# Kernel tuning notes

Hardware: AMD Instinct MI355X
Metric: run time of the kernel (lower is better)

The kernel has to match this reference:

```python
import jax, jax.numpy as jnp
import numpy as np

B, L, DIN = 2, 4096, 1024
W = 64            # windowsize
G, H = 8, 8       # groups, heads per group
DQ = DV = 64
FF = 1024
NEG = -1e30


def rmsnorm(x, gamma, d):
    # F.normalize(x, dim=-1) * sqrt(d) * gamma
    n = jnp.sqrt(jnp.sum(x * x, axis=-1, keepdims=True))
    return x / jnp.maximum(n, 1e-12) * (d ** 0.5) * gamma


def setup_inputs() -> dict:
    key = jax.random.key(0)
    ks = jax.random.split(key, 8)
    s = 0.02
    return {
        "x": jax.random.normal(ks[0], (B, L, DIN), jnp.float32),
        "norm_gamma": jnp.ones((DIN,), jnp.float32),
        "Wq_w": jax.random.normal(ks[1], (G * H * DQ, DIN), jnp.float32) * s,
        "Wq_b": jnp.zeros((G * H * DQ,), jnp.float32),
        "Wkv_w": jax.random.normal(ks[2], (G * (DQ + DV), DIN), jnp.float32) * s,
        "Wkv_b": jnp.zeros((G * (DQ + DV),), jnp.float32),
        "wz_gamma1": jnp.ones((G * H * DV,), jnp.float32),
        "W1_w": jax.random.normal(ks[3], (2 * FF, G * H * DV), jnp.float32) * s,
        "W1_b": jnp.zeros((2 * FF,), jnp.float32),
        "wz_gamma2": jnp.ones((2 * FF,), jnp.float32),
        "W2_w": jax.random.normal(ks[4], (FF, 2 * FF), jnp.float32) * s,
        "W2_b": jnp.zeros((FF,), jnp.float32),
    }


def reference(x, norm_gamma, Wq_w, Wq_b, Wkv_w, Wkv_b,
              wz_gamma1, W1_w, W1_b, wz_gamma2, W2_w, W2_b):
    w2, w4 = W // 2, W // 4
    S = 2 * L // W  # number of query chunks (L % W == 0 -> drop_last path)

    xn = rmsnorm(x, norm_gamma, DIN)
    q = xn @ Wq_w.T + Wq_b          # [B, L, G*H*DQ]
    kv = xn @ Wkv_w.T + Wkv_b       # [B, L, G*(DQ+DV)]

    # pad_to_multiple(kv, W, mod=W//2): L % W == 0 -> append W//2 zeros
    kv = jnp.pad(kv, ((0, 0), (0, w2), (0, 0)))
    k, v = jnp.split(kv, 2, axis=-1)  # each [B, L+W/2, G*DQ]
    # F.pad W//4 both sides, then overlapping windows of size W, stride W//2
    k = jnp.pad(k, ((0, 0), (w4, w4), (0, 0)))  # [B, L+W, G*DQ]
    v = jnp.pad(v, ((0, 0), (w4, w4), (0, 0)))
    idx = jnp.arange(S)[:, None] * w2 + jnp.arange(W)[None, :]  # [S, W] (drop_last applied)
    kwin = k[:, idx].reshape(B, S, W, G, DQ).transpose(0, 3, 1, 2, 4)  # [B,G,S,W,DQ]
    vwin = v[:, idx].reshape(B, S, W, G, DV).transpose(0, 3, 1, 2, 4)  # [B,G,S,W,DV]

    # 'B (S w) (G H D) -> B G H S w D'
    qh = q.reshape(B, S, w2, G, H, DQ).transpose(0, 3, 4, 1, 2, 5)  # [B,G,H,S,w2,DQ]

    qk = jnp.einsum('bghsqd,bgskd->bghsqk', qh, kwin) * (1.0 / DQ ** 0.5)
    # edge masking: first chunk can't see left pad, last chunk can't see right pad
    maskb = jnp.zeros((S, W), bool).at[0, :w4].set(True).at[S - 1, W - w4:].set(True)
    qk = jnp.where(maskb[None, None, None, :, None, :], NEG, qk)
    attn = jax.nn.softmax(qk, axis=-1)
    o = jnp.einsum('bghsqk,bgskd->bghsqd', attn, vwin)
    o = o.transpose(0, 3, 4, 1, 2, 5).reshape(B, L, G * H * DV)  # 'B G H S w D -> B (S w) (G H D)'

    # Wz: RMSNorm -> Linear -> SiLU -> RMSNorm -> Linear -> SiLU (dropout=0)
    z = rmsnorm(o, wz_gamma1, G * H * DV)
    z = jax.nn.silu(z @ W1_w.T + W1_b)
    z = rmsnorm(z, wz_gamma2, 2 * FF)
    z = jax.nn.silu(z @ W2_w.T + W2_b)
    return z
```

## Files before the change

### kernel.cpp

```cpp
#include <hip/hip_runtime.h>
#include <cstdint>

typedef _Float16 f16;
typedef f16 f16x4 __attribute__((ext_vector_type(4)));
typedef f16 f16x8 __attribute__((ext_vector_type(8)));
typedef float f32x4 __attribute__((ext_vector_type(4)));

#define MFMA16(a, b, c) __builtin_amdgcn_mfma_f32_16x16x32_f16(a, b, c, 0, 0, 0)

static __device__ __forceinline__ void gload16(const void* g, void* l) {
    __builtin_amdgcn_global_load_lds(
        (const __attribute__((address_space(1))) uint32_t*)g,
        (__attribute__((address_space(3))) uint32_t*)l, 16, 0, 0);
}

template <int NM, int ND, int NV>
static __device__ __forceinline__ void sgb_phase() {
    if (NV > 0) __builtin_amdgcn_sched_group_barrier(0x10, NV, 0);
    constexpr int PER = NM / ND;
#pragma unroll
    for (int i = 0; i < ND; ++i) {
        __builtin_amdgcn_sched_group_barrier(0x8, PER, 0);
        __builtin_amdgcn_sched_group_barrier(0x100, 1, 0);
    }
    if (NM - PER * ND > 0)
        __builtin_amdgcn_sched_group_barrier(0x8, NM - PER * ND, 0);
}

static __device__ __forceinline__ float blockReduceSum256(float v) {
    __shared__ float red[4];
#pragma unroll
    for (int off = 32; off > 0; off >>= 1) v += __shfl_xor(v, off);
    if ((threadIdx.x & 63) == 0) red[threadIdx.x >> 6] = v;
    __syncthreads();
    return red[0] + red[1] + red[2] + red[3];
}

__global__ __launch_bounds__(256) void k_rmsnorm_x(const float* __restrict__ x,
                                                   const float* __restrict__ gamma,
                                                   f16* __restrict__ out) {
    size_t row = blockIdx.x;
    const float4 v = reinterpret_cast<const float4*>(x + row * 1024)[threadIdx.x];
    float ss = v.x * v.x + v.y * v.y + v.z * v.z + v.w * v.w;
    ss = blockReduceSum256(ss);
    float sc = 32.0f / fmaxf(sqrtf(ss), 1e-12f);
    const float4 g = reinterpret_cast<const float4*>(gamma)[threadIdx.x];
    f16x4 o;
    o[0] = (f16)(v.x * sc * g.x); o[1] = (f16)(v.y * sc * g.y);
    o[2] = (f16)(v.z * sc * g.z); o[3] = (f16)(v.w * sc * g.w);
    *reinterpret_cast<f16x4*>(out + row * 1024 + threadIdx.x * 4) = o;
}

template <int D>
__global__ __launch_bounds__(256) void k_rowss(const f16* __restrict__ in,
                                               float* __restrict__ sc) {
    constexpr int PER = D / 256;
    size_t row = blockIdx.x;
    const f16* ir = in + row * D;
    int c0 = threadIdx.x * PER;
    float ss = 0.f;
#pragma unroll
    for (int i = 0; i < PER; i += 8) {
        f16x8 h = *reinterpret_cast<const f16x8*>(ir + c0 + i);
#pragma unroll
        for (int e = 0; e < 8; ++e) { float f = (float)h[e]; ss += f * f; }
    }
    ss = blockReduceSum256(ss);
    if (threadIdx.x == 0)
        sc[row] = sqrtf((float)D) / fmaxf(sqrtf(ss), 1e-12f);
}

__global__ __launch_bounds__(256) void k_cast(const float* __restrict__ in,
                                              f16* __restrict__ out, int n4) {
    int i = blockIdx.x * 256 + threadIdx.x;
    if (i >= n4) return;
    float4 v = reinterpret_cast<const float4*>(in)[i];
    f16x4 o; o[0] = (f16)v.x; o[1] = (f16)v.y; o[2] = (f16)v.z; o[3] = (f16)v.w;
    *reinterpret_cast<f16x4*>(out + (size_t)i * 4) = o;
}

__global__ __launch_bounds__(256) void k_cast_g(const float* __restrict__ in,
                                                f16* __restrict__ out,
                                                const float* __restrict__ gamma,
                                                int kmask, int n4) {
    int i = blockIdx.x * 256 + threadIdx.x;
    if (i >= n4) return;
    float4 v = reinterpret_cast<const float4*>(in)[i];
    int e0 = (i * 4) & kmask;
    f16x4 o;
    o[0] = (f16)(v.x * gamma[e0]); o[1] = (f16)(v.y * gamma[e0 + 1]);
    o[2] = (f16)(v.z * gamma[e0 + 2]); o[3] = (f16)(v.w * gamma[e0 + 3]);
    *reinterpret_cast<f16x4*>(out + (size_t)i * 4) = o;
}

__global__ __launch_bounds__(256) void k_bias_cat(const float* __restrict__ a,
                                                  const float* __restrict__ b,
                                                  float* __restrict__ o) {
    int i = blockIdx.x * 256 + threadIdx.x;
    o[i] = (i < 4096) ? a[i] : b[i - 4096];
}

template <int BN, int EPI, int MODE>
__global__ __launch_bounds__(512, 2) void k_gemm8p(const f16* __restrict__ A,
                                                   const f16* __restrict__ Bt,
                                                   const float* __restrict__ bias,
                                                   const float* __restrict__ rowsc,
                                                   void* __restrict__ Cout,
                                                   int M, int N, int K) {
    constexpr int BM = 256;
    constexpr int WN = BN / 64, WM = 8 / WN, WR = BM / WM;
    constexpr int MW = WR / 16, MH = MW / 2;
    constexpr int LA = 2, LB = BN / 128;
    constexpr int VS = 2 * LA + LB;
    constexpr int AK = BM * 32;
    constexpr int BKE = BN * 32;
    constexpr int SE = 2 * AK + 2 * BKE;

    __shared__ alignas(16) f16 lds[2 * SE];

    const int nb = N / BN;
    int bn, bm;
    if (MODE == 0) { bn = blockIdx.x & 7; bm = blockIdx.x >> 3; }
    else           { bn = blockIdx.x % nb; bm = blockIdx.x / nb; }

    const int tid = threadIdx.x, w = tid >> 6, l = tid & 63;
    const int wm = w / WN, wn = w % WN;
    const int lrow = l & 15, lq = l >> 4;
    const int g = (lrow >> 1) & 3;

    const f16* Ab = A + (size_t)bm * BM * K;
    const f16* Bb = Bt + (size_t)bn * BN * K;
    const int NT = K >> 6;

    int aoff[MW], boff[4];
#pragma unroll
    for (int m = 0; m < MW; ++m)
        aoff[m] = (wm * WR + m * 16 + lrow) * 32 + 8 * (lq ^ g);
#pragma unroll
    for (int n = 0; n < 4; ++n)
        boff[n] = (wn * 64 + n * 16 + lrow) * 32 + 8 * (lq ^ g);

    auto stageA = [&](int k0, f16* region) {
#pragma unroll
        for (int q = 0; q < LA; ++q) {
            int r = q * 128 + w * 16 + (l >> 2);
            int c = 8 * ((l & 3) ^ ((r >> 1) & 3));
            gload16(Ab + (size_t)r * K + k0 + c, region + q * 4096 + w * 512);
        }
    };
    auto stageB = [&](int k0, f16* region) {
#pragma unroll
        for (int q = 0; q < LB; ++q) {
            int r = q * 128 + w * 16 + (l >> 2);
            int c = 8 * ((l & 3) ^ ((r >> 1) & 3));
            gload16(Bb + (size_t)r * K + k0 + c, region + q * 4096 + w * 512);
        }
    };
    auto rdA = [&](f16x8 (&d)[MH], const f16* base, int h) {
#pragma unroll
        for (int m = 0; m < MH; ++m)
            d[m] = *reinterpret_cast<const f16x8*>(base + aoff[h * MH + m]);
    };
    auto rdB = [&](f16x8 (&d)[4], const f16* base) {
#pragma unroll
        for (int n = 0; n < 4; ++n)
            d[n] = *reinterpret_cast<const f16x8*>(base + boff[n]);
    };

    f32x4 acc[MW][4] = {};
    f16x8 afA[MH], afB[MH], bfA[4], bfB[4];

    auto mfmaLo = [&](f16x8 (&af)[MH], f16x8 (&bf)[4]) {
#pragma unroll
        for (int m = 0; m < MH; ++m)
#pragma unroll
            for (int n = 0; n < 4; ++n)
                acc[m][n] = MFMA16(af[m], bf[n], acc[m][n]);
    };
    auto mfmaHi = [&](f16x8 (&af)[MH], f16x8 (&bf)[4]) {
#pragma unroll
        for (int m = 0; m < MH; ++m)
#pragma unroll
            for (int n = 0; n < 4; ++n)
                acc[MH + m][n] = MFMA16(af[m], bf[n], acc[MH + m][n]);
    };

    stageA(0, lds);             stageB(0, lds + 2 * AK);
    stageA(32, lds + AK);       stageB(32, lds + 2 * AK + BKE);
    stageA(64, lds + SE);       stageB(64, lds + SE + 2 * AK);
    asm volatile("s_waitcnt vmcnt(%0)" :: "i"(2 * (LA + LB)) : "memory");
    __builtin_amdgcn_s_barrier();
    rdA(afA, lds, 0);
    rdB(bfA, lds + 2 * AK);

    const int NTm2 = NT - 2;
    for (int t = 0; t < NTm2; ++t) {
        f16* s0 = lds + (t & 1) * SE;
        f16* s1 = lds + ((t & 1) ^ 1) * SE;
        const int kn1 = (t + 1) << 6;
        const int kn2 = (t + 2) << 6;
        __builtin_amdgcn_s_barrier();
        stageA(kn1 + 32, s1 + AK);
        rdA(afB, s0, 1);
        mfmaLo(afA, bfA);
        sgb_phase<MH * 4, MH, LA>();
        asm volatile("s_waitcnt vmcnt(%0)" :: "i"(VS) : "memory");
        __builtin_amdgcn_s_barrier();
        stageB(kn1 + 32, s1 + 2 * AK + BKE);
        rdA(afA, s0 + AK, 0);
        rdB(bfB, s0 + 2 * AK + BKE);
        mfmaHi(afB, bfA);
        sgb_phase<MH * 4, MH + 4, LB>();
        __builtin_amdgcn_s_barrier();
        stageA(kn2, s0);
        rdA(afB, s0 + AK, 1);
        mfmaLo(afA, bfB);
        sgb_phase<MH * 4, MH, LA>();
        asm volatile("s_waitcnt vmcnt(%0)" :: "i"(VS) : "memory");
        __builtin_amdgcn_s_barrier();
        stageB(kn2, s0 + 2 * AK);
        rdA(afA, s1, 0);
        rdB(bfA, s1 + 2 * AK);
        mfmaHi(afB, bfB);
        sgb_phase<MH * 4, MH + 4, LB>();
    }
    {
        const int t = NTm2;
        f16* s0 = lds + (t & 1) * SE;
        f16* s1 = lds + ((t & 1) ^ 1) * SE;
        const int kn1 = (t + 1) << 6;
        __builtin_amdgcn_s_barrier();
        stageA(kn1 + 32, s1 + AK);
        rdA(afB, s0, 1);
        mfmaLo(afA, bfA);
        sgb_phase<MH * 4, MH, LA>();
        asm volatile("s_waitcnt vmcnt(%0)" :: "i"(VS) : "memory");
        __builtin_amdgcn_s_barrier();
        stageB(kn1 + 32, s1 + 2 * AK + BKE);
        rdA(afA, s0 + AK, 0);
        rdB(bfB, s0 + 2 * AK + BKE);
        mfmaHi(afB, bfA);
        sgb_phase<MH * 4, MH + 4, LB>();
        __builtin_amdgcn_s_barrier();
        rdA(afB, s0 + AK, 1);
        mfmaLo(afA, bfB);
        sgb_phase<MH * 4, MH, 0>();
        asm volatile("s_waitcnt vmcnt(%0)" :: "i"(LA + LB) : "memory");
        __builtin_amdgcn_s_barrier();
        rdA(afA, s1, 0);
        rdB(bfA, s1 + 2 * AK);
        mfmaHi(afB, bfB);
        sgb_phase<MH * 4, MH + 4, 0>();
    }
    {
        f16* s0 = lds + ((NT - 1) & 1) * SE;
        __builtin_amdgcn_s_barrier();
        rdA(afB, s0, 1);
        mfmaLo(afA, bfA);
        sgb_phase<MH * 4, MH, 0>();
        asm volatile("s_waitcnt vmcnt(0)" ::: "memory");
        __builtin_amdgcn_s_barrier();
        rdA(afA, s0 + AK, 0);
        rdB(bfB, s0 + 2 * AK + BKE);
        mfmaHi(afB, bfA);
        sgb_phase<MH * 4, MH + 4, 0>();
        __builtin_amdgcn_s_barrier();
        rdA(afB, s0 + AK, 1);
        mfmaLo(afA, bfB);
        sgb_phase<MH * 4, MH, 0>();
        mfmaHi(afB, bfB);
    }

    const size_t row0 = (size_t)bm * BM + wm * WR;
    const int col0 = bn * BN + wn * 64;
    float bsv[4];
#pragma unroll
    for (int n = 0; n < 4; ++n) bsv[n] = bias[col0 + n * 16 + lrow];
#pragma unroll
    for (int m = 0; m < MW; ++m) {
#pragma unroll
        for (int r = 0; r < 4; ++r) {
            const size_t row = row0 + m * 16 + lq * 4 + r;
            float scl = (EPI >= 1) ? rowsc[row] : 1.0f;
#pragma unroll
            for (int n = 0; n < 4; ++n) {
                float v = acc[m][n][r];
                if (EPI >= 1) v = v * scl;
                v += bsv[n];
                if (EPI >= 1) v = v / (1.f + __expf(-v));
                const size_t idx = row * N + col0 + n * 16 + lrow;
                if (EPI == 2) reinterpret_cast<float*>(Cout)[idx] = v;
                else          reinterpret_cast<f16*>(Cout)[idx] = (f16)v;
            }
        }
    }
}

__global__ __launch_bounds__(256) void k_attn(const f16* __restrict__ qkv,
                                              f16* __restrict__ o) {
    __shared__ alignas(16) f16 Ksm[64 * 64];
    __shared__ alignas(16) f16 Vtsm[64 * 64];
    __shared__ alignas(16) f16 Psm[4][64 * 64];
    const int idx = blockIdx.x;
    const int s = idx & 127;
    const int g = (idx >> 7) & 7;
    const int b = idx >> 10;
    const int tid = threadIdx.x;
    const int w = tid >> 6, l = tid & 63;

    const int baseR = s * 32 - 16;
#pragma unroll
    for (int i = 0; i < 2; ++i) {
        const int j = i * 32 + (tid >> 3);
        const int d0 = (tid & 7) * 8;
        const int R = baseR + j;
        f16x8 kvv = {}, vvv = {};
        if (R >= 0 && R < 4096) {
            const f16* rp = qkv + ((size_t)(b * 4096 + R)) * 5120 + 4096 + g * 64 + d0;
            kvv = *reinterpret_cast<const f16x8*>(rp);
            vvv = *reinterpret_cast<const f16x8*>(rp + 512);
        }
        *reinterpret_cast<f16x8*>(&Ksm[j * 64 + d0]) = kvv;
#pragma unroll
        for (int e = 0; e < 8; ++e) Vtsm[(d0 + e) * 64 + j] = vvv[e];
    }

    const int lrow = l & 15, lk = (l >> 4) * 8;
    f16x8 aq[4][2];
#pragma unroll
    for (int m = 0; m < 4; ++m) {
        const int qr = w * 64 + m * 16 + lrow;
        const int h = qr >> 5, qi = qr & 31;
        const f16* qp = qkv + ((size_t)(b * 4096 + s * 32 + qi)) * 5120 + (g * 8 + h) * 64 + lk;
        aq[m][0] = *reinterpret_cast<const f16x8*>(qp);
        aq[m][1] = *reinterpret_cast<const f16x8*>(qp + 32);
    }
    __syncthreads();

    f32x4 acc[4][4] = {};
#pragma unroll
    for (int kk = 0; kk < 2; ++kk) {
        f16x8 bk[4];
#pragma unroll
        for (int n = 0; n < 4; ++n)
            bk[n] = *reinterpret_cast<const f16x8*>(&Ksm[(n * 16 + lrow) * 64 + kk * 32 + lk]);
#pragma unroll
        for (int m = 0; m < 4; ++m)
#pragma unroll
            for (int n = 0; n < 4; ++n)
                acc[m][n] = MFMA16(aq[m][kk], bk[n], acc[m][n]);
    }

    const int nlo = (s == 0) ? 1 : 0;
    const int nhi = (s == 127) ? 3 : 4;
#pragma unroll
    for (int m = 0; m < 4; ++m) {
#pragma unroll
        for (int r = 0; r < 4; ++r) {
            float xv[4];
#pragma unroll
            for (int n = 0; n < 4; ++n) xv[n] = acc[m][n][r] * 0.125f;
            float mx = -1e30f;
            for (int n = nlo; n < nhi; ++n) mx = fmaxf(mx, xv[n]);
#pragma unroll
            for (int off = 8; off > 0; off >>= 1) mx = fmaxf(mx, __shfl_xor(mx, off));
            float pv[4]; float sum = 0.f;
#pragma unroll
            for (int n = 0; n < 4; ++n) {
                float e = (n >= nlo && n < nhi) ? __expf(xv[n] - mx) : 0.f;
                pv[n] = e; sum += e;
            }
#pragma unroll
            for (int off = 8; off > 0; off >>= 1) sum += __shfl_xor(sum, off);
            const float inv = 1.f / sum;
            const int prow = m * 16 + (l >> 4) * 4 + r;
#pragma unroll
            for (int n = 0; n < 4; ++n)
                Psm[w][prow * 64 + n * 16 + lrow] = (f16)(pv[n] * inv);
        }
    }
    __syncthreads();

    f32x4 oacc[4][4] = {};
#pragma unroll
    for (int kk = 0; kk < 2; ++kk) {
        f16x8 ap[4], bv[4];
#pragma unroll
        for (int m = 0; m < 4; ++m)
            ap[m] = *reinterpret_cast<const f16x8*>(&Psm[w][(m * 16 + lrow) * 64 + kk * 32 + lk]);
#pragma unroll
        for (int n = 0; n < 4; ++n)
            bv[n] = *reinterpret_cast<const f16x8*>(&Vtsm[(n * 16 + lrow) * 64 + kk * 32 + lk]);
#pragma unroll
        for (int m = 0; m < 4; ++m)
#pragma unroll
            for (int n = 0; n < 4; ++n)
                oacc[m][n] = MFMA16(ap[m], bv[n], oacc[m][n]);
    }
    const int lr4 = (l >> 4) * 4;
#pragma unroll
    for (int m = 0; m < 4; ++m) {
#pragma unroll
        for (int r = 0; r < 4; ++r) {
            const int qr = w * 64 + m * 16 + lr4 + r;
            const int h = qr >> 5, qi = qr & 31;
            f16* op = o + ((size_t)(b * 4096 + s * 32 + qi)) * 4096 + (g * 8 + h) * 64;
#pragma unroll
            for (int n = 0; n < 4; ++n) op[n * 16 + lrow] = (f16)oacc[m][n][r];
        }
    }
}

extern "C" void kernel_launch(void* const* d_in, const int* in_sizes, int n_in,
                              void* d_out, int out_size, void* d_ws, size_t ws_size,
                              hipStream_t stream) {
    const float* x     = (const float*)d_in[0];
    const float* ng    = (const float*)d_in[1];
    const float* Wq_w  = (const float*)d_in[2];
    const float* Wq_b  = (const float*)d_in[3];
    const float* Wkv_w = (const float*)d_in[4];
    const float* Wkv_b = (const float*)d_in[5];
    const float* g1    = (const float*)d_in[6];
    const float* W1_w  = (const float*)d_in[7];
    const float* W1_b  = (const float*)d_in[8];
    const float* g2    = (const float*)d_in[9];
    const float* W2_w  = (const float*)d_in[10];
    const float* W2_b  = (const float*)d_in[11];
    float* out = (float*)d_out;

    char* p = (char*)d_ws;
    f16* qkv  = (f16*)(p);
    f16* h1   = (f16*)(p);
    f16* xn   = (f16*)(p + 83886080);
    f16* ob   = (f16*)(p + 83886080);
    f16* w1   = (f16*)(p + 150994944);
    f16* w2   = (f16*)(p + 167772160);
    f16* wqkv = (f16*)(p + 171966464);
    float* cb  = (float*)(p + 182452224);
    float* sc1 = (float*)(p + 182472704);
    float* sc2 = (float*)(p + 182505472);

    k_cast<<<4096, 256, 0, stream>>>(Wq_w, wqkv, 4096 * 1024 / 4);
    k_cast<<<1024, 256, 0, stream>>>(Wkv_w, wqkv + 4096 * 1024, 1024 * 1024 / 4);
    k_cast_g<<<8192, 256, 0, stream>>>(W1_w, w1, g1, 4095, 2048 * 4096 / 4);
    k_cast_g<<<2048, 256, 0, stream>>>(W2_w, w2, g2, 2047, 1024 * 2048 / 4);
    k_bias_cat<<<20, 256, 0, stream>>>(Wq_b, Wkv_b, cb);
    k_rmsnorm_x<<<8192, 256, 0, stream>>>(x, ng, xn);

    k_gemm8p<256, 0, 1><<<640, 512, 0, stream>>>(xn, wqkv, cb, nullptr, qkv, 8192, 5120, 1024);

    k_attn<<<2048, 256, 0, stream>>>(qkv, ob);

    k_rowss<4096><<<8192, 256, 0, stream>>>(ob, sc1);
    k_gemm8p<256, 1, 0><<<256, 512, 0, stream>>>(ob, w1, W1_b, sc1, h1, 8192, 2048, 4096);
    k_rowss<2048><<<8192, 256, 0, stream>>>(h1, sc2);
    k_gemm8p<128, 2, 0><<<256, 512, 0, stream>>>(h1, w2, W2_b, sc2, (void*)out, 8192, 1024, 2048);

    (void)in_sizes; (void)n_in; (void)out_size; (void)ws_size;
}
```

Before: 371.9 us.

## Fuse row sum-of-squares into producer epilogues and merge weight-prep kernels

Drops the two standalone row-norm kernels. The attention and first GEMM epilogues now accumulate each row's sum of squares with wave shuffles and atomicAdd, and the consuming GEMM turns that into the RMSNorm scale. The weight casts, bias concat and zeroing of the accumulators are merged into one prep launch. This saves re-reading the 64MB and 32MB intermediates and several launches, at the cost of atomic contention and sums computed from fp32 values rather than the rounded f16 ones.

```diff
diff --git a/kernel.cpp b/kernel.cpp
--- a/kernel.cpp
+++ b/kernel.cpp
@@ -51,60 +51,58 @@
     *reinterpret_cast<f16x4*>(out + row * 1024 + threadIdx.x * 4) = o;
 }
 
-template <int D>
-__global__ __launch_bounds__(256) void k_rowss(const f16* __restrict__ in,
-                                               float* __restrict__ sc) {
-    constexpr int PER = D / 256;
-    size_t row = blockIdx.x;
-    const f16* ir = in + row * D;
-    int c0 = threadIdx.x * PER;
-    float ss = 0.f;
-#pragma unroll
-    for (int i = 0; i < PER; i += 8) {
-        f16x8 h = *reinterpret_cast<const f16x8*>(ir + c0 + i);
-#pragma unroll
-        for (int e = 0; e < 8; ++e) { float f = (float)h[e]; ss += f * f; }
-    }
-    ss = blockReduceSum256(ss);
-    if (threadIdx.x == 0)
-        sc[row] = sqrtf((float)D) / fmaxf(sqrtf(ss), 1e-12f);
-}
-
-__global__ __launch_bounds__(256) void k_cast(const float* __restrict__ in,
-                                              f16* __restrict__ out, int n4) {
+__global__ __launch_bounds__(256) void k_prep(
+    const float* __restrict__ Wq_w, const float* __restrict__ Wkv_w,
+    const float* __restrict__ W1_w, const float* __restrict__ g1,
+    const float* __restrict__ W2_w, const float* __restrict__ g2,
+    const float* __restrict__ Wq_b, const float* __restrict__ Wkv_b,
+    f16* __restrict__ wqkv, f16* __restrict__ w1, f16* __restrict__ w2,
+    float* __restrict__ cb, float* __restrict__ scz) {
     int i = blockIdx.x * 256 + threadIdx.x;
-    if (i >= n4) return;
-    float4 v = reinterpret_cast<const float4*>(in)[i];
-    f16x4 o; o[0] = (f16)v.x; o[1] = (f16)v.y; o[2] = (f16)v.z; o[3] = (f16)v.w;
-    *reinterpret_cast<f16x4*>(out + (size_t)i * 4) = o;
-}
-
-__global__ __launch_bounds__(256) void k_cast_g(const float* __restrict__ in,
-                                                f16* __restrict__ out,
-                                                const float* __restrict__ gamma,
-                                                int kmask, int n4) {
-    int i = blockIdx.x * 256 + threadIdx.x;
-    if (i >= n4) return;
-    float4 v = reinterpret_cast<const float4*>(in)[i];
-    int e0 = (i * 4) & kmask;
-    f16x4 o;
-    o[0] = (f16)(v.x * gamma[e0]); o[1] = (f16)(v.y * gamma[e0 + 1]);
-    o[2] = (f16)(v.z * gamma[e0 + 2]); o[3] = (f16)(v.w * gamma[e0 + 3]);
-    *reinterpret_cast<f16x4*>(out + (size_t)i * 4) = o;
-}
-
-__global__ __launch_bounds__(256) void k_bias_cat(const float* __restrict__ a,
-                                                  const float* __restrict__ b,
-                                                  float* __restrict__ o) {
-    int i = blockIdx.x * 256 + threadIdx.x;
-    o[i] = (i < 4096) ? a[i] : b[i - 4096];
+    if (i < 1048576) {
+        float4 v = reinterpret_cast<const float4*>(Wq_w)[i];
+        f16x4 o; o[0] = (f16)v.x; o[1] = (f16)v.y; o[2] = (f16)v.z; o[3] = (f16)v.w;
+        *reinterpret_cast<f16x4*>(wqkv + (size_t)i * 4) = o;
+    } else if (i < 1310720) {
+        int j = i - 1048576;
+        float4 v = reinterpret_cast<const float4*>(Wkv_w)[j];
+        f16x4 o; o[0] = (f16)v.x; o[1] = (f16)v.y; o[2] = (f16)v.z; o[3] = (f16)v.w;
+        *reinterpret_cast<f16x4*>(wqkv + 4194304 + (size_t)j * 4) = o;
+    } else if (i < 3407872) {
+        int j = i - 1310720;
+        float4 v = reinterpret_cast<const float4*>(W1_w)[j];
+        int c = (j * 4) & 4095;
+        f16x4 o;
+        o[0] = (f16)(v.x * g1[c]);     o[1] = (f16)(v.y * g1[c + 1]);
+        o[2] = (f16)(v.z * g1[c + 2]); o[3] = (f16)(v.w * g1[c + 3]);
+        *reinterpret_cast<f16x4*>(w1 + (size_t)j * 4) = o;
+    } else if (i < 3932160) {
+        int j = i - 3407872;
+        float4 v = reinterpret_cast<const float4*>(W2_w)[j];
+        int c = (j * 4) & 2047;
+        f16x4 o;
+        o[0] = (f16)(v.x * g2[c]);     o[1] = (f16)(v.y * g2[c + 1]);
+        o[2] = (f16)(v.z * g2[c + 2]); o[3] = (f16)(v.w * g2[c + 3]);
+        *reinterpret_cast<f16x4*>(w2 + (size_t)j * 4) = o;
+    } else if (i < 3933440) {
+        int j = i - 3932160;
+        int e = j * 4;
+        float4 o4 = (e < 4096) ? reinterpret_cast<const float4*>(Wq_b)[j]
+                               : reinterpret_cast<const float4*>(Wkv_b)[(e - 4096) >> 2];
+        reinterpret_cast<float4*>(cb)[j] = o4;
+    } else if (i < 3937536) {
+        int j = i - 3933440;
+        reinterpret_cast<float4*>(scz)[j] = make_float4(0.f, 0.f, 0.f, 0.f);
+    }
 }
 
 template <int BN, int EPI, int MODE>
 __global__ __launch_bounds__(512, 2) void k_gemm8p(const f16* __restrict__ A,
                                                    const f16* __restrict__ Bt,
                                                    const float* __restrict__ bias,
-                                                   const float* __restrict__ rowsc,
+                                                   const float* __restrict__ ssin,
+                                                   float sqrtD,
+                                                   float* __restrict__ ssout,
                                                    void* __restrict__ Cout,
                                                    int M, int N, int K) {
     constexpr int BM = 256;
@@ -281,23 +279,35 @@
 #pragma unroll
         for (int r = 0; r < 4; ++r) {
             const size_t row = row0 + m * 16 + lq * 4 + r;
-            float scl = (EPI >= 1) ? rowsc[row] : 1.0f;
+            float scl = 1.0f;
+            if (EPI >= 1)
+                scl = sqrtD / fmaxf(sqrtf(ssin[row]), 1e-12f);
+            float ssp = 0.f;
 #pragma unroll
             for (int n = 0; n < 4; ++n) {
                 float v = acc[m][n][r];
                 if (EPI >= 1) v = v * scl;
                 v += bsv[n];
                 if (EPI >= 1) v = v / (1.f + __expf(-v));
+                if (EPI == 1) ssp += v * v;
                 const size_t idx = row * N + col0 + n * 16 + lrow;
                 if (EPI == 2) reinterpret_cast<float*>(Cout)[idx] = v;
                 else          reinterpret_cast<f16*>(Cout)[idx] = (f16)v;
             }
+            if (EPI == 1) {
+                ssp += __shfl_xor(ssp, 1);
+                ssp += __shfl_xor(ssp, 2);
+                ssp += __shfl_xor(ssp, 4);
+                ssp += __shfl_xor(ssp, 8);
+                if (lrow == 0) atomicAdd(&ssout[row], ssp);
+            }
         }
     }
 }
 
 __global__ __launch_bounds__(256) void k_attn(const f16* __restrict__ qkv,
-                                              f16* __restrict__ o) {
+                                              f16* __restrict__ o,
+                                              float* __restrict__ ssout) {
     __shared__ alignas(16) f16 Ksm[64 * 64];
     __shared__ alignas(16) f16 Vtsm[64 * 64];
     __shared__ alignas(16) f16 Psm[4][64 * 64];
@@ -405,8 +415,19 @@
             const int qr = w * 64 + m * 16 + lr4 + r;
             const int h = qr >> 5, qi = qr & 31;
             f16* op = o + ((size_t)(b * 4096 + s * 32 + qi)) * 4096 + (g * 8 + h) * 64;
-#pragma unroll
-            for (int n = 0; n < 4; ++n) op[n * 16 + lrow] = (f16)oacc[m][n][r];
+            float ssp = 0.f;
+#pragma unroll
+            for (int n = 0; n < 4; ++n) {
+                float v = oacc[m][n][r];
+                op[n * 16 + lrow] = (f16)v;
+                ssp += v * v;
+            }
+            ssp += __shfl_xor(ssp, 1);
+            ssp += __shfl_xor(ssp, 2);
+            ssp += __shfl_xor(ssp, 4);
+            ssp += __shfl_xor(ssp, 8);
+            if (lrow == 0)
+                atomicAdd(&ssout[(size_t)(b * 4096 + s * 32 + qi)], ssp);
         }
     }
 }
@@ -440,21 +461,19 @@
     float* sc1 = (float*)(p + 182472704);
     float* sc2 = (float*)(p + 182505472);
 
-    k_cast<<<4096, 256, 0, stream>>>(Wq_w, wqkv, 4096 * 1024 / 4);
-    k_cast<<<1024, 256, 0, stream>>>(Wkv_w, wqkv + 4096 * 1024, 1024 * 1024 / 4);
-    k_cast_g<<<8192, 256, 0, stream>>>(W1_w, w1, g1, 4095, 2048 * 4096 / 4);
-    k_cast_g<<<2048, 256, 0, stream>>>(W2_w, w2, g2, 2047, 1024 * 2048 / 4);
-    k_bias_cat<<<20, 256, 0, stream>>>(Wq_b, Wkv_b, cb);
+    k_prep<<<15381, 256, 0, stream>>>(Wq_w, Wkv_w, W1_w, g1, W2_w, g2, Wq_b, Wkv_b,
+                                      wqkv, w1, w2, cb, sc1);
     k_rmsnorm_x<<<8192, 256, 0, stream>>>(x, ng, xn);
 
-    k_gemm8p<256, 0, 1><<<640, 512, 0, stream>>>(xn, wqkv, cb, nullptr, qkv, 8192, 5120, 1024);
-
-    k_attn<<<2048, 256, 0, stream>>>(qkv, ob);
-
-    k_rowss<4096><<<8192, 256, 0, stream>>>(ob, sc1);
-    k_gemm8p<256, 1, 0><<<256, 512, 0, stream>>>(ob, w1, W1_b, sc1, h1, 8192, 2048, 4096);
-    k_rowss<2048><<<8192, 256, 0, stream>>>(h1, sc2);
-    k_gemm8p<128, 2, 0><<<256, 512, 0, stream>>>(h1, w2, W2_b, sc2, (void*)out, 8192, 1024, 2048);
+    k_gemm8p<256, 0, 1><<<640, 512, 0, stream>>>(xn, wqkv, cb, nullptr, 0.f, nullptr,
+                                                 qkv, 8192, 5120, 1024);
+
+    k_attn<<<2048, 256, 0, stream>>>(qkv, ob, sc1);
+
+    k_gemm8p<256, 1, 0><<<256, 512, 0, stream>>>(ob, w1, W1_b, sc1, 64.0f, sc2,
+                                                 h1, 8192, 2048, 4096);
+    k_gemm8p<128, 2, 0><<<256, 512, 0, stream>>>(h1, w2, W2_b, sc2, 45.254834f, nullptr,
+                                                 (void*)out, 8192, 1024, 2048);
 
     (void)in_sizes; (void)n_in; (void)out_size; (void)ws_size;
 }
```

Result: no change. 370.2 us (-0.5%).
